# Kernel optimization log

Hardware: AMD Instinct MI355X
Metric: run time of the kernel (lower is better)

Reference implementation:

```python
import jax, jax.numpy as jnp
import numpy as np

BS, H = 2048, 1024
XDIM = 2048 + 4 * 64  # x + R*W = 2304
IN = XDIM + 2 * H     # 4352


def setup_inputs() -> dict:
    key = jax.random.key(0)
    ks = jax.random.split(key, 11)
    s = 1.0 / np.sqrt(IN)  # torch Linear default init scale
    return {
        "input_x": jax.random.normal(ks[0], (BS, XDIM), jnp.float32),
        "previous_time": jax.random.normal(ks[1], (BS, H), jnp.float32),
        "previous_layer": jax.random.normal(ks[2], (BS, H), jnp.float32),
        "old_state": jnp.zeros((BS, H), jnp.float32),
        "Wi": jax.random.normal(ks[3], (H, IN), jnp.float32) * s,
        "bi": jax.random.normal(ks[4], (H,), jnp.float32) * s,
        "Wf": jax.random.normal(ks[5], (H, IN), jnp.float32) * s,
        "bf": jax.random.normal(ks[6], (H,), jnp.float32) * s,
        "Wo": jax.random.normal(ks[7], (H, IN), jnp.float32) * s,
        "bo": jax.random.normal(ks[8], (H,), jnp.float32) * s,
        "Ws": jax.random.normal(ks[9], (H, IN), jnp.float32) * s,
        "bs_state": jax.random.normal(ks[10], (H,), jnp.float32) * s,
    }


def reference(input_x, previous_time, previous_layer, old_state,
              Wi, bi, Wf, bf, Wo, bo, Ws, bs_state):
    # semicolon_input: [bs, x + R*W + 2h]
    z = jnp.concatenate([input_x, previous_time, previous_layer], axis=1)
    # Fuse the four projections into one GEMM: [bs, 4h]
    W_all = jnp.concatenate([Wi, Wf, Wo, Ws], axis=0)          # [4h, IN]
    b_all = jnp.concatenate([bi, bf, bo, bs_state], axis=0)    # [4h]
    proj = z @ W_all.T + b_all
    gi, gf, go, gs = jnp.split(proj, 4, axis=1)
    input_gate = jax.nn.sigmoid(gi)
    forget_gate = jax.nn.sigmoid(gf)
    output_gate = jax.nn.sigmoid(go)
    new_state = forget_gate * old_state + input_gate * jnp.tanh(gs)
    new_hidden = output_gate * jnp.tanh(new_state)
    return new_hidden
```

## Files before the change

### kernel.cpp

```cpp
#include <hip/hip_runtime.h>
#include <stdint.h>
#include <stddef.h>

#define M_DIM 2048
#define N_DIM 4096
#define K_DIM 4352
#define H_DIM 1024
#define X_DIM 2304

#define A_OFF 0u
#define B_OFF 17825792u

typedef __bf16 bf16x8 __attribute__((ext_vector_type(8)));
typedef float f32x4 __attribute__((ext_vector_type(4)));

__device__ __forceinline__ unsigned short f32_to_bf16(float f) {
    unsigned u = __float_as_uint(f);
    u += 0x7FFFu + ((u >> 16) & 1u);
    return (unsigned short)(u >> 16);
}

__device__ __forceinline__ float sigm_(float x) { return 1.f / (1.f + __expf(-x)); }
__device__ __forceinline__ float tanh_(float x) {
    x = fminf(15.f, fmaxf(-15.f, x));
    float e = __expf(2.f * x);
    return (e - 1.f) / (e + 1.f);
}

__global__ __launch_bounds__(256) void convert_kernel(
    const float* __restrict__ x, const float* __restrict__ pt,
    const float* __restrict__ pl,
    const float* __restrict__ Wi, const float* __restrict__ Wf,
    const float* __restrict__ Wo, const float* __restrict__ Ws,
    unsigned short* __restrict__ Abf, unsigned short* __restrict__ Bbf)
{
    const int row = blockIdx.x;
    const float* srow = nullptr;
    unsigned short* drow;
    if (row < M_DIM) {
        drow = Abf + (size_t)row * K_DIM;
    } else {
        int n = row - M_DIM;
        int g = n >> 10, h = n & 1023;
        const float* W = (g == 0) ? Wi : (g == 1) ? Wf : (g == 2) ? Wo : Ws;
        srow = W + (size_t)h * K_DIM;
        drow = Bbf + (size_t)(h * 4 + g) * K_DIM;
    }

    for (int c8 = threadIdx.x; c8 < K_DIM / 8; c8 += 256) {
        int col = c8 * 8;
        const float* s;
        if (row < M_DIM) {
            if (col < X_DIM)              s = x  + (size_t)row * X_DIM + col;
            else if (col < X_DIM + H_DIM) s = pt + (size_t)row * H_DIM + (col - X_DIM);
            else                          s = pl + (size_t)row * H_DIM + (col - X_DIM - H_DIM);
        } else {
            s = srow + col;
        }
        float4 v0 = ((const float4*)s)[0];
        float4 v1 = ((const float4*)s)[1];
        union { unsigned short h[8]; uint4 u; } r;
        r.h[0] = f32_to_bf16(v0.x); r.h[1] = f32_to_bf16(v0.y);
        r.h[2] = f32_to_bf16(v0.z); r.h[3] = f32_to_bf16(v0.w);
        r.h[4] = f32_to_bf16(v1.x); r.h[5] = f32_to_bf16(v1.y);
        r.h[6] = f32_to_bf16(v1.z); r.h[7] = f32_to_bf16(v1.w);
        *(uint4*)(drow + col) = r.u;
    }
}

__global__ __launch_bounds__(512, 2) void gemm_fused(
    const unsigned short* __restrict__ A,
    const unsigned short* __restrict__ B,
    const float* __restrict__ old_state,
    const float* __restrict__ bi, const float* __restrict__ bfv,
    const float* __restrict__ bo, const float* __restrict__ bs,
    float* __restrict__ out)
{
    __shared__ __align__(16) char smem[98304];
    float* sP = (float*)smem;

    const int tid  = threadIdx.x;
    const int lane = tid & 63;
    const int wave = tid >> 6;
    const int wm = (wave >> 2) * 64;
    const int wn = (wave & 3) * 64;

    const int b   = blockIdx.x;
    const int xcd = b & 7;
    const int j   = b >> 3;
    const int m0  = (j >> 1) * 128;
    const int n0  = (xcd * 2 + (j & 1)) * 256;

    const int srow_ = tid >> 2;
    const int kb_   = (tid & 3) ^ ((tid >> 3) & 3);
    const unsigned short* Asrc  = A + (size_t)(m0 + srow_)       * K_DIM + kb_ * 8;
    const unsigned short* Bsrc0 = B + (size_t)(n0 + srow_)       * K_DIM + kb_ * 8;
    const unsigned short* Bsrc1 = B + (size_t)(n0 + 128 + srow_) * K_DIM + kb_ * 8;

    const int fr  = lane & 15;
    const int kb0 = lane >> 4;
    const int swz = (kb0 ^ ((fr >> 1) & 3)) * 16;
    const int aoff = (wm + fr) * 64 + swz;
    const int boff = 8192 + (wn + fr) * 64 + swz;

    f32x4 acc[4][4];
#pragma unroll
    for (int i = 0; i < 4; ++i)
#pragma unroll
        for (int jj = 0; jj < 4; ++jj) acc[i][jj] = (f32x4){0.f, 0.f, 0.f, 0.f};

    auto stage = [&](int h, int c) {
        const size_t koff = (size_t)h * 32;
        __builtin_amdgcn_global_load_lds(
            (const __attribute__((address_space(1))) unsigned*)(Asrc + koff),
            (__attribute__((address_space(3))) unsigned*)(smem + c * 24576 + wave * 1024),
            16, 0, 0);
        __builtin_amdgcn_global_load_lds(
            (const __attribute__((address_space(1))) unsigned*)(Bsrc0 + koff),
            (__attribute__((address_space(3))) unsigned*)(smem + c * 24576 + 8192 + wave * 1024),
            16, 0, 0);
        __builtin_amdgcn_global_load_lds(
            (const __attribute__((address_space(1))) unsigned*)(Bsrc1 + koff),
            (__attribute__((address_space(3))) unsigned*)(smem + c * 24576 + 16384 + wave * 1024),
            16, 0, 0);
    };

#define VM3 asm volatile("s_waitcnt vmcnt(3)" ::: "memory")
#define VM0 asm volatile("s_waitcnt vmcnt(0)" ::: "memory")
#define VMNONE ((void)0)

#define PHASE(C, SH, DOSTAGE, VMLINE)                                           \
    do {                                                                        \
        if (DOSTAGE) stage((SH), ((C) + 2) & 3);                                \
        bf16x8 af[4], bq[4];                                                    \
        _Pragma("unroll")                                                       \
        for (int i_ = 0; i_ < 4; ++i_) {                                        \
            af[i_] = *(const bf16x8*)(smem + (C) * 24576 + aoff + i_ * 1024);   \
            bq[i_] = *(const bf16x8*)(smem + (C) * 24576 + boff + i_ * 1024);   \
        }                                                                       \
        VMLINE;                                                                 \
        __builtin_amdgcn_s_barrier();                                           \
        __builtin_amdgcn_s_setprio(1);                                          \
        _Pragma("unroll")                                                       \
        for (int i_ = 0; i_ < 4; ++i_)                                          \
            _Pragma("unroll")                                                   \
            for (int j_ = 0; j_ < 4; ++j_)                                      \
                acc[i_][j_] = __builtin_amdgcn_mfma_f32_16x16x32_bf16(          \
                    af[i_], bq[j_], acc[i_][j_], 0, 0, 0);                      \
        __builtin_amdgcn_s_setprio(0);                                          \
    } while (0)

    stage(0, 0); stage(1, 1);
    VM3;
    __builtin_amdgcn_s_barrier();

    for (int h4 = 0; h4 < 132; h4 += 4) {
        PHASE(0, h4 + 2, true, VM3);
        PHASE(1, h4 + 3, true, VM3);
        PHASE(2, h4 + 4, true, VM3);
        PHASE(3, h4 + 5, true, VM3);
    }
    PHASE(0, 134, true,  VM3);
    PHASE(1, 135, true,  VM3);
    PHASE(2, 0,   false, VM0);
    PHASE(3, 0,   false, VMNONE);

#undef PHASE
#undef VM3
#undef VM0
#undef VMNONE

    const int cw = lane & 15;
    const int rw = (lane >> 4) * 4;
    const int hl = tid & 15;
    const int rb = tid >> 4;

    for (int p = 0; p < 4; ++p) {
        __syncthreads();
        if ((wave & 3) == p) {
#pragma unroll
            for (int i = 0; i < 4; ++i)
#pragma unroll
                for (int jj = 0; jj < 4; ++jj)
#pragma unroll
                    for (int r = 0; r < 4; ++r)
                        sP[(wm + i * 16 + rw + r) * 76 + jj * 16 + cw] = acc[i][jj][r];
        }
        __syncthreads();

        const int hg = (n0 >> 2) + p * 16 + hl;
        const float b_i = bi[hg], b_f = bfv[hg], b_o = bo[hg], b_s = bs[hg];
#pragma unroll
        for (int k = 0; k < 4; ++k) {
            const int row = rb + 32 * k;
            float4 g = *(const float4*)(sP + row * 76 + hl * 4);
            const size_t oidx = (size_t)(m0 + row) * H_DIM + hg;
            float old = old_state[oidx];
            float ig = sigm_(g.x + b_i);
            float fg = sigm_(g.y + b_f);
            float og = sigm_(g.z + b_o);
            float ts = tanh_(g.w + b_s);
            out[oidx] = og * tanh_(fg * old + ig * ts);
        }
    }
}

extern "C" void kernel_launch(void* const* d_in, const int* in_sizes, int n_in,
                              void* d_out, int out_size, void* d_ws, size_t ws_size,
                              hipStream_t stream) {
    const float* x   = (const float*)d_in[0];
    const float* pt  = (const float*)d_in[1];
    const float* pl  = (const float*)d_in[2];
    const float* old = (const float*)d_in[3];
    const float* Wi  = (const float*)d_in[4];
    const float* bi  = (const float*)d_in[5];
    const float* Wf  = (const float*)d_in[6];
    const float* bf  = (const float*)d_in[7];
    const float* Wo  = (const float*)d_in[8];
    const float* bo  = (const float*)d_in[9];
    const float* Ws  = (const float*)d_in[10];
    const float* bs  = (const float*)d_in[11];
    float* out = (float*)d_out;

    char* ws = (char*)d_ws;
    unsigned short* Abf = (unsigned short*)(ws + A_OFF);
    unsigned short* Bbf = (unsigned short*)(ws + B_OFF);

    convert_kernel<<<M_DIM + N_DIM, 256, 0, stream>>>(x, pt, pl, Wi, Wf, Wo, Ws, Abf, Bbf);

    gemm_fused<<<256, 512, 0, stream>>>(Abf, Bbf, old, bi, bf, bo, bs, out);
}
```

Measured before the change: 231.1 us.

## Software-pipeline LDS fragment reads one stage ahead of MFMAs with register double-buffering

Restructures the GEMM main loop so each phase loads the next k-slice's A/B fragments from LDS into alternate register sets while the MFMAs run on the current set, with sched_barriers fixing the order. Global prefetch depth rises from two to three stages of the four-buffer ring, and the barrier now comes after the MFMAs. The aim is to hide LDS read latency and barrier stalls behind matrix math, at the cost of more live VGPRs and a hand-checked buffer-reuse schedule.

```diff
diff --git a/kernel.cpp b/kernel.cpp
--- a/kernel.cpp
+++ b/kernel.cpp
@@ -125,47 +125,59 @@
             16, 0, 0);
     };
 
+    bf16x8 a0[4], b0[4], a1[4], b1[4];
+
 #define VM3 asm volatile("s_waitcnt vmcnt(3)" ::: "memory")
 #define VM0 asm volatile("s_waitcnt vmcnt(0)" ::: "memory")
 #define VMNONE ((void)0)
 
-#define PHASE(C, SH, DOSTAGE, VMLINE)                                           \
+#define READS(AN, BN, NBUF)                                                     \
+    _Pragma("unroll")                                                           \
+    for (int i_ = 0; i_ < 4; ++i_) {                                            \
+        AN[i_] = *(const bf16x8*)(smem + (NBUF) * 24576 + aoff + i_ * 1024);    \
+        BN[i_] = *(const bf16x8*)(smem + (NBUF) * 24576 + boff + i_ * 1024);    \
+    }
+
+#define MFMAS(AC, BC)                                                           \
+    __builtin_amdgcn_s_setprio(1);                                              \
+    _Pragma("unroll")                                                           \
+    for (int i_ = 0; i_ < 4; ++i_)                                              \
+        _Pragma("unroll")                                                       \
+        for (int j_ = 0; j_ < 4; ++j_)                                          \
+            acc[i_][j_] = __builtin_amdgcn_mfma_f32_16x16x32_bf16(              \
+                AC[i_], BC[j_], acc[i_][j_], 0, 0, 0);                          \
+    __builtin_amdgcn_s_setprio(0);
+
+#define PHASE(AC, BC, AN, BN, NBUF, SH, DOSTAGE, VMLINE, DOBAR)                 \
     do {                                                                        \
-        if (DOSTAGE) stage((SH), ((C) + 2) & 3);                                \
-        bf16x8 af[4], bq[4];                                                    \
-        _Pragma("unroll")                                                       \
-        for (int i_ = 0; i_ < 4; ++i_) {                                        \
-            af[i_] = *(const bf16x8*)(smem + (C) * 24576 + aoff + i_ * 1024);   \
-            bq[i_] = *(const bf16x8*)(smem + (C) * 24576 + boff + i_ * 1024);   \
-        }                                                                       \
+        READS(AN, BN, NBUF);                                                    \
+        if (DOSTAGE) stage((SH), (SH) & 3);                                     \
+        __builtin_amdgcn_sched_barrier(0);                                      \
+        MFMAS(AC, BC);                                                          \
+        __builtin_amdgcn_sched_barrier(0);                                      \
         VMLINE;                                                                 \
-        __builtin_amdgcn_s_barrier();                                           \
-        __builtin_amdgcn_s_setprio(1);                                          \
-        _Pragma("unroll")                                                       \
-        for (int i_ = 0; i_ < 4; ++i_)                                          \
-            _Pragma("unroll")                                                   \
-            for (int j_ = 0; j_ < 4; ++j_)                                      \
-                acc[i_][j_] = __builtin_amdgcn_mfma_f32_16x16x32_bf16(          \
-                    af[i_], bq[j_], acc[i_][j_], 0, 0, 0);                      \
-        __builtin_amdgcn_s_setprio(0);                                          \
+        if (DOBAR) __builtin_amdgcn_s_barrier();                                \
     } while (0)
 
-    stage(0, 0); stage(1, 1);
+    stage(0, 0); stage(1, 1); stage(2, 2);
     VM3;
     __builtin_amdgcn_s_barrier();
-
-    for (int h4 = 0; h4 < 132; h4 += 4) {
-        PHASE(0, h4 + 2, true, VM3);
-        PHASE(1, h4 + 3, true, VM3);
-        PHASE(2, h4 + 4, true, VM3);
-        PHASE(3, h4 + 5, true, VM3);
-    }
-    PHASE(0, 134, true,  VM3);
-    PHASE(1, 135, true,  VM3);
-    PHASE(2, 0,   false, VM0);
-    PHASE(3, 0,   false, VMNONE);
+    READS(a0, b0, 0);
+
+    for (int p4 = 0; p4 < 132; p4 += 4) {
+        PHASE(a0, b0, a1, b1, 1, p4 + 3, true, VM3, true);
+        PHASE(a1, b1, a0, b0, 2, p4 + 4, true, VM3, true);
+        PHASE(a0, b0, a1, b1, 3, p4 + 5, true, VM3, true);
+        PHASE(a1, b1, a0, b0, 0, p4 + 6, true, VM3, true);
+    }
+    PHASE(a0, b0, a1, b1, 1, 135, true,  VM3,    true);
+    PHASE(a1, b1, a0, b0, 2, 0,   false, VM0,    true);
+    PHASE(a0, b0, a1, b1, 3, 0,   false, VMNONE, false);
+    MFMAS(a1, b1);
 
 #undef PHASE
+#undef READS
+#undef MFMAS
 #undef VM3
 #undef VM0
 #undef VMNONE
```

After: 233.0 us. About the same (+0.8%).

## Load B fragments directly to registers, stage only A through LDS

Applied to the files above, without the earlier changes.

Restructures the GEMM main loop so that only the A tile goes through LDS, using a double buffer with a 64-wide K step. B fragments are loaded straight from global memory into registers with register double buffering. This shrinks LDS use from 96KB to 40KB and removes the B LDS round trip. In exchange, B loads are no longer shared across the two M-waves, which doubles B global traffic per block. It also raises register pressure and replaces the 4-stage pipeline with a 2-stage one using full syncthreads.

```diff
diff --git a/kernel.cpp b/kernel.cpp
--- a/kernel.cpp
+++ b/kernel.cpp
@@ -76,7 +76,7 @@
     const float* __restrict__ bo, const float* __restrict__ bs,
     float* __restrict__ out)
 {
-    __shared__ __align__(16) char smem[98304];
+    __shared__ __align__(16) char smem[40960];
     float* sP = (float*)smem;
 
     const int tid  = threadIdx.x;
@@ -91,17 +91,20 @@
     const int m0  = (j >> 1) * 128;
     const int n0  = (xcd * 2 + (j & 1)) * 256;
 
-    const int srow_ = tid >> 2;
-    const int kb_   = (tid & 3) ^ ((tid >> 3) & 3);
-    const unsigned short* Asrc  = A + (size_t)(m0 + srow_)       * K_DIM + kb_ * 8;
-    const unsigned short* Bsrc0 = B + (size_t)(n0 + srow_)       * K_DIM + kb_ * 8;
-    const unsigned short* Bsrc1 = B + (size_t)(n0 + 128 + srow_) * K_DIM + kb_ * 8;
+    const int arow = tid >> 3;
+    const int akb  = (tid & 7) ^ ((tid >> 3) & 7);
+    const unsigned short* Asrc = A + (size_t)(m0 + arow) * K_DIM + akb * 8;
 
     const int fr  = lane & 15;
     const int kb0 = lane >> 4;
-    const int swz = (kb0 ^ ((fr >> 1) & 3)) * 16;
-    const int aoff = (wm + fr) * 64 + swz;
-    const int boff = 8192 + (wn + fr) * 64 + swz;
+    const int aRowByte = (wm + fr) * 128;
+    const int sA0 = ((kb0     ) ^ (fr & 7)) << 4;
+    const int sA1 = ((kb0 ^ 4 ) ^ (fr & 7)) << 4;
+
+    const unsigned short* Bp[4];
+#pragma unroll
+    for (int q = 0; q < 4; ++q)
+        Bp[q] = B + (size_t)(n0 + wn + q * 16 + fr) * K_DIM + kb0 * 8;
 
     f32x4 acc[4][4];
 #pragma unroll
@@ -109,66 +112,59 @@
 #pragma unroll
         for (int jj = 0; jj < 4; ++jj) acc[i][jj] = (f32x4){0.f, 0.f, 0.f, 0.f};
 
-    auto stage = [&](int h, int c) {
-        const size_t koff = (size_t)h * 32;
-        __builtin_amdgcn_global_load_lds(
-            (const __attribute__((address_space(1))) unsigned*)(Asrc + koff),
-            (__attribute__((address_space(3))) unsigned*)(smem + c * 24576 + wave * 1024),
+    bf16x8 bCur[8], bNxt[8];
+
+#define STAGE_A(P, BUF)                                                         \
+    _Pragma("unroll")                                                           \
+    for (int i_ = 0; i_ < 2; ++i_)                                              \
+        __builtin_amdgcn_global_load_lds(                                       \
+            (const __attribute__((address_space(1))) unsigned*)                 \
+                (Asrc + (size_t)i_ * 64 * K_DIM + (size_t)(P) * 64),            \
+            (__attribute__((address_space(3))) unsigned*)                       \
+                (smem + (BUF) + i_ * 8192 + wave * 1024),                       \
             16, 0, 0);
-        __builtin_amdgcn_global_load_lds(
-            (const __attribute__((address_space(1))) unsigned*)(Bsrc0 + koff),
-            (__attribute__((address_space(3))) unsigned*)(smem + c * 24576 + 8192 + wave * 1024),
-            16, 0, 0);
-        __builtin_amdgcn_global_load_lds(
-            (const __attribute__((address_space(1))) unsigned*)(Bsrc1 + koff),
-            (__attribute__((address_space(3))) unsigned*)(smem + c * 24576 + 16384 + wave * 1024),
-            16, 0, 0);
-    };
-
-#define VM3 asm volatile("s_waitcnt vmcnt(3)" ::: "memory")
-#define VM0 asm volatile("s_waitcnt vmcnt(0)" ::: "memory")
-#define VMNONE ((void)0)
-
-#define PHASE(C, SH, DOSTAGE, VMLINE)                                           \
+
+#define PREFETCH_B(BB, P)                                                       \
+    _Pragma("unroll")                                                           \
+    for (int q_ = 0; q_ < 8; ++q_)                                              \
+        BB[q_] = *(const bf16x8*)(Bp[q_ & 3] + (size_t)(P) * 64 + (q_ >> 2) * 32);
+
+#define COMPUTE(BUF, BB)                                                        \
     do {                                                                        \
-        if (DOSTAGE) stage((SH), ((C) + 2) & 3);                                \
-        bf16x8 af[4], bq[4];                                                    \
+        bf16x8 af_[4];                                                          \
         _Pragma("unroll")                                                       \
-        for (int i_ = 0; i_ < 4; ++i_) {                                        \
-            af[i_] = *(const bf16x8*)(smem + (C) * 24576 + aoff + i_ * 1024);   \
-            bq[i_] = *(const bf16x8*)(smem + (C) * 24576 + boff + i_ * 1024);   \
+        for (int kh_ = 0; kh_ < 2; ++kh_) {                                     \
+            _Pragma("unroll")                                                   \
+            for (int i_ = 0; i_ < 4; ++i_)                                      \
+                af_[i_] = *(const bf16x8*)(smem + (BUF) + aRowByte + i_ * 2048  \
+                                           + (kh_ ? sA1 : sA0));                \
+            _Pragma("unroll")                                                   \
+            for (int i_ = 0; i_ < 4; ++i_)                                      \
+                _Pragma("unroll")                                               \
+                for (int j_ = 0; j_ < 4; ++j_)                                  \
+                    acc[i_][j_] = __builtin_amdgcn_mfma_f32_16x16x32_bf16(      \
+                        af_[i_], BB[kh_ * 4 + j_], acc[i_][j_], 0, 0, 0);       \
         }                                                                       \
-        VMLINE;                                                                 \
-        __builtin_amdgcn_s_barrier();                                           \
-        __builtin_amdgcn_s_setprio(1);                                          \
-        _Pragma("unroll")                                                       \
-        for (int i_ = 0; i_ < 4; ++i_)                                          \
-            _Pragma("unroll")                                                   \
-            for (int j_ = 0; j_ < 4; ++j_)                                      \
-                acc[i_][j_] = __builtin_amdgcn_mfma_f32_16x16x32_bf16(          \
-                    af[i_], bq[j_], acc[i_][j_], 0, 0, 0);                      \
-        __builtin_amdgcn_s_setprio(0);                                          \
     } while (0)
 
-    stage(0, 0); stage(1, 1);
-    VM3;
-    __builtin_amdgcn_s_barrier();
-
-    for (int h4 = 0; h4 < 132; h4 += 4) {
-        PHASE(0, h4 + 2, true, VM3);
-        PHASE(1, h4 + 3, true, VM3);
-        PHASE(2, h4 + 4, true, VM3);
-        PHASE(3, h4 + 5, true, VM3);
-    }
-    PHASE(0, 134, true,  VM3);
-    PHASE(1, 135, true,  VM3);
-    PHASE(2, 0,   false, VM0);
-    PHASE(3, 0,   false, VMNONE);
-
-#undef PHASE
-#undef VM3
-#undef VM0
-#undef VMNONE
+    STAGE_A(0, 0);
+    PREFETCH_B(bCur, 0);
+    __syncthreads();
+
+    for (int p = 0; p < 68; p += 2) {
+        if (p + 1 < 68) { PREFETCH_B(bNxt, p + 1); STAGE_A(p + 1, 16384); }
+        __builtin_amdgcn_sched_barrier(0);
+        COMPUTE(0, bCur);
+        __syncthreads();
+        if (p + 2 < 68) { PREFETCH_B(bCur, p + 2); STAGE_A(p + 2, 0); }
+        __builtin_amdgcn_sched_barrier(0);
+        COMPUTE(16384, bNxt);
+        __syncthreads();
+    }
+
+#undef STAGE_A
+#undef PREFETCH_B
+#undef COMPUTE
 
     const int cw = lane & 15;
     const int rw = (lane >> 4) * 4;
```

New measurement: 322.2 us. 39.4% more time.
